# Optimization experiments

Hardware: AMD Instinct MI355X
Metric: run time of the kernel (lower is better)

The kernel has to match this reference:

```python
import jax, jax.numpy as jnp
import numpy as np

N_NODES = 100000
N_EDGES = 3200000


def setup_inputs() -> dict:
    key = jax.random.key(0)
    ks = jax.random.split(key, 5)
    features = jax.random.normal(ks[0], (N_NODES, 1433), dtype=jnp.float32)
    src = jax.random.randint(ks[1], (N_EDGES,), 0, N_NODES, dtype=jnp.int32)
    dst = jax.random.randint(ks[2], (N_EDGES,), 0, N_NODES, dtype=jnp.int32)
    # Glorot-ish init for weights
    W1 = jax.random.normal(ks[3], (1433, 16), dtype=jnp.float32) * (1.0 / np.sqrt(1433))
    W2 = jax.random.normal(ks[4], (16, 7), dtype=jnp.float32) * (1.0 / np.sqrt(16))
    b1 = jnp.zeros((16,), dtype=jnp.float32)
    b2 = jnp.zeros((7,), dtype=jnp.float32)
    return {"features": features, "src": src, "dst": dst,
            "W1": W1, "b1": b1, "W2": W2, "b2": b2}


def _degree_norms(src, dst, n_nodes, dtype):
    ones = jnp.ones(src.shape[0], dtype=dtype)
    deg_out = jax.ops.segment_sum(ones, src, num_segments=n_nodes)
    deg_in = jax.ops.segment_sum(ones, dst, num_segments=n_nodes)
    # DGL clamps zero degrees to 1
    norm_src = jax.lax.rsqrt(jnp.maximum(deg_out, 1.0))
    norm_dst = jax.lax.rsqrt(jnp.maximum(deg_in, 1.0))
    return norm_src, norm_dst


def _graph_conv(x, W, b, src, dst, norm_src, norm_dst, n_nodes):
    # DGL GraphConv, norm='both', in_feats > out_feats => weight applied first
    h = (x * norm_src[:, None]) @ W            # [N, out]
    agg = jax.ops.segment_sum(h[src], dst, num_segments=n_nodes)  # scatter-add over edges
    return agg * norm_dst[:, None] + b


def reference(features, src, dst, W1, b1, W2, b2):
    n_nodes = features.shape[0]
    norm_src, norm_dst = _degree_norms(src, dst, n_nodes, features.dtype)
    h = _graph_conv(features, W1, b1, src, dst, norm_src, norm_dst, n_nodes)
    h = jax.nn.relu(h)  # layer-1 activation (relu applied twice in original; idempotent)
    out = _graph_conv(h, W2, b2, src, dst, norm_src, norm_dst, n_nodes)
    return out
```

## Files before the change

kernel.cpp:

```cpp
#include <hip/hip_runtime.h>
#include <math.h>

#define N_NODES  100000
#define N_EDGES  3200000
#define K_IN     1433
#define NH       16
#define NO       7

#define TK       16
#define KSPLIT   9
#define CPS      10
#define RW       (CPS * TK)
#define TILE_R   128
#define SXS      20
#define NTILEV   ((N_NODES + TILE_R - 1) / TILE_R)
#define NRBV     ((NTILEV + 3) / 4)
#define SLOT     96

#define NBKT     256
#define BKN      391
#define SBLK     512
#define EPB      ((N_EDGES + SBLK - 1) / SBLK)

typedef float f4  __attribute__((ext_vector_type(4)));
typedef float f4u __attribute__((ext_vector_type(4), aligned(4)));

__global__ __launch_bounds__(256)
void k_pcount(const int* __restrict__ key, int* __restrict__ partial) {
    __shared__ int lh[NBKT];
    lh[threadIdx.x] = 0;
    __syncthreads();
    const int e0 = blockIdx.x * EPB;
    const int e1 = min(e0 + EPB, N_EDGES);
    for (int i = e0 + threadIdx.x; i < e1; i += 256)
        atomicAdd(&lh[key[i] / BKN], 1);
    __syncthreads();
    partial[blockIdx.x * NBKT + threadIdx.x] = lh[threadIdx.x];
}

__global__ __launch_bounds__(256)
void k_colscan(const int* __restrict__ partial, int* __restrict__ pbase,
               int* __restrict__ btot) {
    __shared__ int s[256];
    const int b = blockIdx.x, t = threadIdx.x;
    const int v0 = partial[(2 * t)     * NBKT + b];
    const int v1 = partial[(2 * t + 1) * NBKT + b];
    const int pair = v0 + v1;
    s[t] = pair;
    __syncthreads();
    for (int o = 1; o < 256; o <<= 1) {
        int u = (t >= o) ? s[t - o] : 0;
        __syncthreads();
        s[t] += u;
        __syncthreads();
    }
    const int excl = s[t] - pair;
    pbase[(2 * t)     * NBKT + b] = excl;
    pbase[(2 * t + 1) * NBKT + b] = excl + v0;
    if (t == 255) btot[b] = s[255];
}

__global__ __launch_bounds__(256)
void k_basescan(const int* __restrict__ btd, int* __restrict__ bbd,
                const int* __restrict__ bts, int* __restrict__ bbs) {
    __shared__ int s[256];
    const int t = threadIdx.x;
    int v = btd[t];
    s[t] = v;
    __syncthreads();
    for (int o = 1; o < 256; o <<= 1) {
        int u = (t >= o) ? s[t - o] : 0;
        __syncthreads();
        s[t] += u;
        __syncthreads();
    }
    bbd[t] = s[t] - v;
    __syncthreads();
    v = bts[t];
    s[t] = v;
    __syncthreads();
    for (int o = 1; o < 256; o <<= 1) {
        int u = (t >= o) ? s[t - o] : 0;
        __syncthreads();
        s[t] += u;
        __syncthreads();
    }
    bbs[t] = s[t] - v;
}

__global__ __launch_bounds__(256)
void k_pscatter2(const int* __restrict__ src, const int* __restrict__ dst,
                 const int* __restrict__ pbase, const int* __restrict__ bbase,
                 int2* __restrict__ ebuf) {
    __shared__ int lh[NBKT];
    __shared__ int lb[NBKT];
    const int t = threadIdx.x;
    lh[t] = 0;
    lb[t] = bbase[t] + pbase[blockIdx.x * NBKT + t];
    __syncthreads();
    const int e0 = blockIdx.x * EPB;
    const int e1 = min(e0 + EPB, N_EDGES);
    for (int i = e0 + t; i < e1; i += 256) {
        int sv = src[i], dv = dst[i];
        int b = dv / BKN;
        int p = lb[b] + atomicAdd(&lh[b], 1);
        ebuf[p] = make_int2(sv, dv);
    }
}

__global__ __launch_bounds__(256)
void k_pscatter1(const int* __restrict__ src, const int* __restrict__ pbase,
                 const int* __restrict__ bbase, int* __restrict__ sbuf) {
    __shared__ int lh[NBKT];
    __shared__ int lb[NBKT];
    const int t = threadIdx.x;
    lh[t] = 0;
    lb[t] = bbase[t] + pbase[blockIdx.x * NBKT + t];
    __syncthreads();
    const int e0 = blockIdx.x * EPB;
    const int e1 = min(e0 + EPB, N_EDGES);
    for (int i = e0 + t; i < e1; i += 256) {
        int sv = src[i];
        int b = sv / BKN;
        int p = lb[b] + atomicAdd(&lh[b], 1);
        sbuf[p] = sv;
    }
}

__global__ __launch_bounds__(512)
void k_adj(const int2* __restrict__ ebuf, const int* __restrict__ bbase,
           const int* __restrict__ btot, int* __restrict__ adj,
           int* __restrict__ cnt) {
    __shared__ int cur[BKN];
    const int b = blockIdx.x;
    for (int i = threadIdx.x; i < BKN; i += 512) cur[i] = 0;
    __syncthreads();
    const int s0 = bbase[b], s1 = s0 + btot[b];
    const int nb = b * BKN;
    for (int i = s0 + threadIdx.x; i < s1; i += 512) {
        int2 e = ebuf[i];
        int p = atomicAdd(&cur[e.y - nb], 1);
        if (p < SLOT) adj[e.y * SLOT + p] = e.x;
    }
    __syncthreads();
    for (int i = threadIdx.x; i < BKN; i += 512) {
        int n = nb + i;
        if (n < N_NODES) cnt[n] = cur[i];
    }
}

__global__ __launch_bounds__(512)
void k_hist(const int* __restrict__ sbuf, const int* __restrict__ bbase,
            const int* __restrict__ btot, int* __restrict__ deg) {
    __shared__ int cur[BKN];
    const int b = blockIdx.x;
    for (int i = threadIdx.x; i < BKN; i += 512) cur[i] = 0;
    __syncthreads();
    const int s0 = bbase[b], s1 = s0 + btot[b];
    const int nb = b * BKN;
    for (int i = s0 + threadIdx.x; i < s1; i += 512)
        atomicAdd(&cur[sbuf[i] - nb], 1);
    __syncthreads();
    for (int i = threadIdx.x; i < BKN; i += 512) {
        int n = nb + i;
        if (n < N_NODES) deg[n] = cur[i];
    }
}


#define LOADG(KN, S0,S1,S2,S3,S4,S5,S6,S7)                               \
  { if ((KN) + TK <= K_IN) {                                             \
      S0 = *(const f4u*)(xp0 + (KN)); S1 = *(const f4u*)(xp1 + (KN));    \
      S2 = *(const f4u*)(xp2 + (KN)); S3 = *(const f4u*)(xp3 + (KN));    \
      S4 = *(const f4u*)(xp4 + (KN)); S5 = *(const f4u*)(xp5 + (KN));    \
      S6 = *(const f4u*)(xp6 + (KN)); S7 = *(const f4u*)(xp7 + (KN));    \
    } else {                                                             \
      S0=0.f;S1=0.f;S2=0.f;S3=0.f;S4=0.f;S5=0.f;S6=0.f;S7=0.f;           \
      if (Lq < 2) {                                                      \
        S0 = *(const f4u*)(xp0 + (KN)); S1 = *(const f4u*)(xp1 + (KN));  \
        S2 = *(const f4u*)(xp2 + (KN)); S3 = *(const f4u*)(xp3 + (KN));  \
        S4 = *(const f4u*)(xp4 + (KN)); S5 = *(const f4u*)(xp5 + (KN));  \
        S6 = *(const f4u*)(xp6 + (KN)); S7 = *(const f4u*)(xp7 + (KN));  \
      } else if (Lq == 2) {                                              \
        S0[0] = xp0[(KN)]; S1[0] = xp1[(KN)];                            \
        S2[0] = xp2[(KN)]; S3[0] = xp3[(KN)];                            \
        S4[0] = xp4[(KN)]; S5[0] = xp5[(KN)];                            \
        S6[0] = xp6[(KN)]; S7[0] = xp7[(KN)];                            \
      }                                                                  \
    } }

#define WRITE_SET(S0,S1,S2,S3,S4,S5,S6,S7)                               \
  { *(f4*)(xbw + 0*16*SXS) = S0; *(f4*)(xbw + 1*16*SXS) = S1;            \
    *(f4*)(xbw + 2*16*SXS) = S2; *(f4*)(xbw + 3*16*SXS) = S3;            \
    *(f4*)(xbw + 4*16*SXS) = S4; *(f4*)(xbw + 5*16*SXS) = S5;            \
    *(f4*)(xbw + 6*16*SXS) = S6; *(f4*)(xbw + 7*16*SXS) = S7; }

#define READ_FMA(CC)                                                     \
  { f4 xa0 = *(const f4*)(xra +  0), xa1 = *(const f4*)(xra +  4);       \
    f4 xa2 = *(const f4*)(xra +  8), xa3 = *(const f4*)(xra + 12);       \
    f4 xb0 = *(const f4*)(xrb +  0), xb1 = *(const f4*)(xrb +  4);       \
    f4 xb2 = *(const f4*)(xrb +  8), xb3 = *(const f4*)(xrb + 12);       \
    const float* wb = wlds + (CC) * (TK * NH);                           \
    _Pragma("unroll")                                                    \
    for (int kk = 0; kk < TK; ++kk) {                                    \
      const f4 va = (kk < 4) ? xa0 : (kk < 8) ? xa1 : (kk < 12) ? xa2 : xa3; \
      const f4 vb = (kk < 4) ? xb0 : (kk < 8) ? xb1 : (kk < 12) ? xb2 : xb3; \
      const float xa = va[kk & 3], xb = vb[kk & 3];                      \
      const f4* wr = (const f4*)(wb + kk * NH);                          \
      const f4 w0 = wr[0], w1 = wr[1], w2 = wr[2], w3 = wr[3];           \
      accA0 += xa * w0; accA1 += xa * w1; accA2 += xa * w2; accA3 += xa * w3; \
      accB0 += xb * w0; accB1 += xb * w1; accB2 += xb * w2; accB3 += xb * w3; \
    } }

__global__ __launch_bounds__(256)
void k_gemm1(const float* __restrict__ X, const float* __restrict__ W1,
             float* __restrict__ hpart) {
    __shared__ float wlds[RW * NH];
    __shared__ float sX[4][TILE_R * SXS];
    const int wid = threadIdx.x >> 6;
    const int t   = threadIdx.x & 63;
    const int rb    = blockIdx.x % NRBV;
    const int split = blockIdx.x / NRBV;

    {
        const f4* W1v = (const f4*)W1;
        const int wbase = split * RW;
#pragma unroll
        for (int r = 0; r < 3; ++r) {
            int idx = r * 256 + threadIdx.x;
            if (idx < RW * 4) {
                int krow = wbase + (idx >> 2);
                f4 wv = 0.f;
                if (krow < K_IN) wv = W1v[krow * 4 + (idx & 3)];
                ((f4*)wlds)[idx] = wv;
            }
        }
    }
    __syncthreads();

    const int tile = rb * 4 + wid;
    if (tile >= NTILEV) return;
    const int base = tile * TILE_R;
    const int Lq = t & 3;
    const int Lr = t >> 2;

    const float* xp0 = X + (size_t)min(base + Lr +   0, N_NODES - 1) * K_IN + 4 * Lq;
    const float* xp1 = X + (size_t)min(base + Lr +  16, N_NODES - 1) * K_IN + 4 * Lq;
    const float* xp2 = X + (size_t)min(base + Lr +  32, N_NODES - 1) * K_IN + 4 * Lq;
    const float* xp3 = X + (size_t)min(base + Lr +  48, N_NODES - 1) * K_IN + 4 * Lq;
    const float* xp4 = X + (size_t)min(base + Lr +  64, N_NODES - 1) * K_IN + 4 * Lq;
    const float* xp5 = X + (size_t)min(base + Lr +  80, N_NODES - 1) * K_IN + 4 * Lq;
    const float* xp6 = X + (size_t)min(base + Lr +  96, N_NODES - 1) * K_IN + 4 * Lq;
    const float* xp7 = X + (size_t)min(base + Lr + 112, N_NODES - 1) * K_IN + 4 * Lq;

    float* xbuf = sX[wid];
    float* xbw  = xbuf + Lr * SXS + 4 * Lq;
    const float* xra = xbuf + t * SXS;
    const float* xrb = xbuf + (t + 64) * SXS;

    f4 accA0 = 0.f, accA1 = 0.f, accA2 = 0.f, accA3 = 0.f;
    f4 accB0 = 0.f, accB1 = 0.f, accB2 = 0.f, accB3 = 0.f;

    f4 sP0, sP1, sP2, sP3, sP4, sP5, sP6, sP7;
    f4 sQ0, sQ1, sQ2, sQ3, sQ4, sQ5, sQ6, sQ7;

    const int k0 = split * RW;
    LOADG(k0, sP0, sP1, sP2, sP3, sP4, sP5, sP6, sP7)

#pragma unroll 1
    for (int j = 0; j < CPS / 2; ++j) {
        const int ke = k0 + 2 * j * TK;
        WRITE_SET(sP0, sP1, sP2, sP3, sP4, sP5, sP6, sP7)
        LOADG(ke + TK, sQ0, sQ1, sQ2, sQ3, sQ4, sQ5, sQ6, sQ7)
        __builtin_amdgcn_wave_barrier();
        READ_FMA(2 * j)
        __builtin_amdgcn_wave_barrier();
        WRITE_SET(sQ0, sQ1, sQ2, sQ3, sQ4, sQ5, sQ6, sQ7)
        if (j + 1 < CPS / 2) {
            LOADG(ke + 2 * TK, sP0, sP1, sP2, sP3, sP4, sP5, sP6, sP7)
        }
        __builtin_amdgcn_wave_barrier();
        READ_FMA(2 * j + 1)
        __builtin_amdgcn_wave_barrier();
    }

    const size_t sb = (size_t)split * N_NODES;
    if (base + t < N_NODES) {
        f4* hp = (f4*)(hpart + (sb + base + t) * NH);
        hp[0] = accA0; hp[1] = accA1; hp[2] = accA2; hp[3] = accA3;
    }
    if (base + 64 + t < N_NODES) {
        f4* hp = (f4*)(hpart + (sb + base + 64 + t) * NH);
        hp[0] = accB0; hp[1] = accB1; hp[2] = accB2; hp[3] = accB3;
    }
}

__global__ __launch_bounds__(256)
void k_reduce(const float* __restrict__ hpart, const int* __restrict__ deg_out,
              float* __restrict__ h) {
    int idx = blockIdx.x * 256 + threadIdx.x;
    if (idx >= N_NODES * 4) return;
    f4 a = 0.f;
#pragma unroll
    for (int s = 0; s < KSPLIT; ++s)
        a += ((const f4*)hpart)[(size_t)s * N_NODES * 4 + idx];
    float ns = rsqrtf((float)max(deg_out[idx >> 2], 1));
    ((f4*)h)[idx] = a * ns;
}

__global__ __launch_bounds__(256)
void k_layer1(const float* __restrict__ h, const int* __restrict__ adj,
              const int* __restrict__ cnt, const int* __restrict__ deg_out,
              const float* __restrict__ W2, const float* __restrict__ b1,
              float* __restrict__ g) {
    const int lane = threadIdx.x & 63;
    const int wid  = threadIdx.x >> 6;
    const int d    = blockIdx.x * 4 + wid;
    if (d >= N_NODES) return;
    const int j4 = lane & 3, slot = lane >> 2;
    const int start = d * SLOT;
    const int deg   = min(cnt[d], SLOT);
    const int end   = start + deg;
    f4 agg = 0.f;
    for (int p = start + slot; p < end; p += 16) {
        int s = adj[p];
        agg += ((const f4*)h)[s * 4 + j4];
    }
#pragma unroll
    for (int off = 4; off < 64; off <<= 1) {
        agg[0] += __shfl_xor(agg[0], off);
        agg[1] += __shfl_xor(agg[1], off);
        agg[2] += __shfl_xor(agg[2], off);
        agg[3] += __shfl_xor(agg[3], off);
    }
    __shared__ float st[4][NH];
    const float nd = rsqrtf((float)max(deg, 1));
    if (slot == 0) {
        f4 bb = ((const f4*)b1)[j4];
        f4 tj;
        tj[0] = fmaxf(fmaf(agg[0], nd, bb[0]), 0.f);
        tj[1] = fmaxf(fmaf(agg[1], nd, bb[1]), 0.f);
        tj[2] = fmaxf(fmaf(agg[2], nd, bb[2]), 0.f);
        tj[3] = fmaxf(fmaf(agg[3], nd, bb[3]), 0.f);
        ((f4*)st[wid])[j4] = tj;
    }
    __builtin_amdgcn_wave_barrier();
    float r = 0.f;
    if (lane < NO) {
#pragma unroll
        for (int qq = 0; qq < NH; ++qq)
            r = fmaf(st[wid][qq], W2[qq * NO + lane], r);
    }
    if (lane < 8) {
        float ns = rsqrtf((float)max(deg_out[d], 1));
        g[(size_t)d * 8 + lane] = (lane < NO) ? ns * r : 0.f;
    }
}

__global__ __launch_bounds__(256)
void k_layer2(const float* __restrict__ g, const int* __restrict__ adj,
              const int* __restrict__ cnt, const float* __restrict__ b2,
              float* __restrict__ out) {
    const int lane = threadIdx.x & 63;
    const int wid  = threadIdx.x >> 6;
    const int d    = blockIdx.x * 4 + wid;
    if (d >= N_NODES) return;
    const int o4 = lane & 1, slot = lane >> 1;
    const int start = d * SLOT;
    const int deg   = min(cnt[d], SLOT);
    const int end   = start + deg;
    f4 agg = 0.f;
    for (int p = start + slot; p < end; p += 32) {
        int s = adj[p];
        agg += ((const f4*)g)[s * 2 + o4];
    }
#pragma unroll
    for (int off = 2; off < 64; off <<= 1) {
        agg[0] += __shfl_xor(agg[0], off);
        agg[1] += __shfl_xor(agg[1], off);
        agg[2] += __shfl_xor(agg[2], off);
        agg[3] += __shfl_xor(agg[3], off);
    }
    const int sl = lane >> 2;
    float v0 = __shfl(agg[0], sl);
    float v1 = __shfl(agg[1], sl);
    float v2 = __shfl(agg[2], sl);
    float v3 = __shfl(agg[3], sl);
    int cm = lane & 3;
    float v = (cm == 0) ? v0 : (cm == 1) ? v1 : (cm == 2) ? v2 : v3;
    if (lane < NO) {
        float nd = rsqrtf((float)max(deg, 1));
        out[(size_t)d * NO + lane] = fmaf(v, nd, b2[lane]);
    }
}

extern "C" void kernel_launch(void* const* d_in, const int* in_sizes, int n_in,
                              void* d_out, int out_size, void* d_ws, size_t ws_size,
                              hipStream_t stream) {
    const float* X   = (const float*)d_in[0];
    const int*   src = (const int*)d_in[1];
    const int*   dst = (const int*)d_in[2];
    const float* W1  = (const float*)d_in[3];
    const float* b1  = (const float*)d_in[4];
    const float* W2  = (const float*)d_in[5];
    const float* b2  = (const float*)d_in[6];
    float* out = (float*)d_out;

    char* w = (char*)d_ws;
    float* hpart    = (float*)w;  w += (size_t)KSPLIT * N_NODES * NH * 4;
    float* h        = (float*)w;  w += (size_t)N_NODES * NH * 4;
    float* g        = (float*)w;  w += (size_t)N_NODES * 8 * 4;
    int*   adj      = (int*)w;    w += (size_t)N_NODES * SLOT * 4;
    int*   deg_out_a= (int*)w;    w += (size_t)N_NODES * 4;
    int*   cnt      = (int*)w;    w += (size_t)N_NODES * 4;
    int2*  ebuf     = (int2*)w;   w += (size_t)N_EDGES * 8;
    int*   sbuf     = (int*)w;    w += (size_t)N_EDGES * 4;
    int*   partial_d= (int*)w;    w += (size_t)SBLK * NBKT * 4;
    int*   partial_s= (int*)w;    w += (size_t)SBLK * NBKT * 4;
    int*   pbase_d  = (int*)w;    w += (size_t)SBLK * NBKT * 4;
    int*   pbase_s  = (int*)w;    w += (size_t)SBLK * NBKT * 4;
    int*   btot_d   = (int*)w;    w += NBKT * 4;
    int*   btot_s   = (int*)w;    w += NBKT * 4;
    int*   bbase_d  = (int*)w;    w += NBKT * 4;
    int*   bbase_s  = (int*)w;    w += NBKT * 4;

    k_pcount   <<<SBLK, 256, 0, stream>>>(dst, partial_d);
    k_pcount   <<<SBLK, 256, 0, stream>>>(src, partial_s);
    k_colscan  <<<NBKT, 256, 0, stream>>>(partial_d, pbase_d, btot_d);
    k_colscan  <<<NBKT, 256, 0, stream>>>(partial_s, pbase_s, btot_s);
    k_basescan <<<1,    256, 0, stream>>>(btot_d, bbase_d, btot_s, bbase_s);
    k_pscatter2<<<SBLK, 256, 0, stream>>>(src, dst, pbase_d, bbase_d, ebuf);
    k_pscatter1<<<SBLK, 256, 0, stream>>>(src, pbase_s, bbase_s, sbuf);
    k_adj      <<<NBKT, 512, 0, stream>>>(ebuf, bbase_d, btot_d, adj, cnt);
    k_hist     <<<NBKT, 512, 0, stream>>>(sbuf, bbase_s, btot_s, deg_out_a);

    k_gemm1 <<<NRBV * KSPLIT, 256, 0, stream>>>(X, W1, hpart);
    k_reduce<<<(N_NODES * 4 + 255) / 256, 256, 0, stream>>>(hpart, deg_out_a, h);
    k_layer1<<<(N_NODES + 3) / 4, 256, 0, stream>>>(h, adj, cnt, deg_out_a,
                                                    W2, b1, g);
    k_layer2<<<(N_NODES + 3) / 4, 256, 0, stream>>>(g, adj, cnt, b2, out);
}
```

Measured before the change: 394.1 us.

## Restructure layer-1 GEMM tiling: 32-row wave tiles with wider K chunks

Rewrites the first-layer feature GEMM so each wave handles 32 rows, loading 64-column chunks with 16 lanes per row for more coalesced global reads. It splits the output across lanes (4 output columns per lane, 2 rows each) and changes the K split from 9 to 8 slabs of 192 columns. This should cut the partial-sum traffic the reduce kernel reads and improve the memory access pattern on the dominant 573 MB feature read. In exchange, each lane now reads more LDS per FMA, and the kernel relies on N_NODES being divisible by 32.

```diff
diff --git a/kernel.cpp b/kernel.cpp
--- a/kernel.cpp
+++ b/kernel.cpp
@@ -7,14 +7,12 @@
 #define NH       16
 #define NO       7
 
-#define TK       16
-#define KSPLIT   9
-#define CPS      10
-#define RW       (CPS * TK)
-#define TILE_R   128
-#define SXS      20
-#define NTILEV   ((N_NODES + TILE_R - 1) / TILE_R)
-#define NRBV     ((NTILEV + 3) / 4)
+#define TR2      32
+#define NT2      (N_NODES / TR2)
+#define NRB2     ((NT2 + 3) / 4)
+#define KS2      8
+#define RW2      192
+#define SX2      68
 #define SLOT     96
 
 #define NBKT     256
@@ -168,131 +166,127 @@
 }
 
 
-#define LOADG(KN, S0,S1,S2,S3,S4,S5,S6,S7)                               \
-  { if ((KN) + TK <= K_IN) {                                             \
-      S0 = *(const f4u*)(xp0 + (KN)); S1 = *(const f4u*)(xp1 + (KN));    \
-      S2 = *(const f4u*)(xp2 + (KN)); S3 = *(const f4u*)(xp3 + (KN));    \
-      S4 = *(const f4u*)(xp4 + (KN)); S5 = *(const f4u*)(xp5 + (KN));    \
-      S6 = *(const f4u*)(xp6 + (KN)); S7 = *(const f4u*)(xp7 + (KN));    \
-    } else {                                                             \
-      S0=0.f;S1=0.f;S2=0.f;S3=0.f;S4=0.f;S5=0.f;S6=0.f;S7=0.f;           \
-      if (Lq < 2) {                                                      \
-        S0 = *(const f4u*)(xp0 + (KN)); S1 = *(const f4u*)(xp1 + (KN));  \
-        S2 = *(const f4u*)(xp2 + (KN)); S3 = *(const f4u*)(xp3 + (KN));  \
-        S4 = *(const f4u*)(xp4 + (KN)); S5 = *(const f4u*)(xp5 + (KN));  \
-        S6 = *(const f4u*)(xp6 + (KN)); S7 = *(const f4u*)(xp7 + (KN));  \
-      } else if (Lq == 2) {                                              \
-        S0[0] = xp0[(KN)]; S1[0] = xp1[(KN)];                            \
-        S2[0] = xp2[(KN)]; S3[0] = xp3[(KN)];                            \
-        S4[0] = xp4[(KN)]; S5[0] = xp5[(KN)];                            \
-        S6[0] = xp6[(KN)]; S7[0] = xp7[(KN)];                            \
-      }                                                                  \
+#define LOADX_FULL(KO, S0,S1,S2,S3,S4,S5,S6,S7)                      \
+  { S0 = *(const f4u*)(xrow + 0*4*K_IN + (KO));                      \
+    S1 = *(const f4u*)(xrow + 1*4*K_IN + (KO));                      \
+    S2 = *(const f4u*)(xrow + 2*4*K_IN + (KO));                      \
+    S3 = *(const f4u*)(xrow + 3*4*K_IN + (KO));                      \
+    S4 = *(const f4u*)(xrow + 4*4*K_IN + (KO));                      \
+    S5 = *(const f4u*)(xrow + 5*4*K_IN + (KO));                      \
+    S6 = *(const f4u*)(xrow + 6*4*K_IN + (KO));                      \
+    S7 = *(const f4u*)(xrow + 7*4*K_IN + (KO)); }
+
+#define LOADX_TAIL(KO, S0,S1,S2,S3,S4,S5,S6,S7)                      \
+  { S0=0.f;S1=0.f;S2=0.f;S3=0.f;S4=0.f;S5=0.f;S6=0.f;S7=0.f;         \
+    const int kl_ = (KO) + 4 * Lq;                                   \
+    if (kl_ + 3 < K_IN) {                                            \
+      LOADX_FULL(KO, S0,S1,S2,S3,S4,S5,S6,S7)                        \
+    } else {                                                         \
+      _Pragma("unroll")                                              \
+      for (int m_ = 0; m_ < 4; ++m_)                                 \
+        if (kl_ + m_ < K_IN) {                                       \
+          S0[m_] = xrow[0*4*K_IN + (KO) + m_];                       \
+          S1[m_] = xrow[1*4*K_IN + (KO) + m_];                       \
+          S2[m_] = xrow[2*4*K_IN + (KO) + m_];                       \
+          S3[m_] = xrow[3*4*K_IN + (KO) + m_];                       \
+          S4[m_] = xrow[4*4*K_IN + (KO) + m_];                       \
+          S5[m_] = xrow[5*4*K_IN + (KO) + m_];                       \
+          S6[m_] = xrow[6*4*K_IN + (KO) + m_];                       \
+          S7[m_] = xrow[7*4*K_IN + (KO) + m_];                       \
+        }                                                            \
     } }
 
-#define WRITE_SET(S0,S1,S2,S3,S4,S5,S6,S7)                               \
-  { *(f4*)(xbw + 0*16*SXS) = S0; *(f4*)(xbw + 1*16*SXS) = S1;            \
-    *(f4*)(xbw + 2*16*SXS) = S2; *(f4*)(xbw + 3*16*SXS) = S3;            \
-    *(f4*)(xbw + 4*16*SXS) = S4; *(f4*)(xbw + 5*16*SXS) = S5;            \
-    *(f4*)(xbw + 6*16*SXS) = S6; *(f4*)(xbw + 7*16*SXS) = S7; }
-
-#define READ_FMA(CC)                                                     \
-  { f4 xa0 = *(const f4*)(xra +  0), xa1 = *(const f4*)(xra +  4);       \
-    f4 xa2 = *(const f4*)(xra +  8), xa3 = *(const f4*)(xra + 12);       \
-    f4 xb0 = *(const f4*)(xrb +  0), xb1 = *(const f4*)(xrb +  4);       \
-    f4 xb2 = *(const f4*)(xrb +  8), xb3 = *(const f4*)(xrb + 12);       \
-    const float* wb = wlds + (CC) * (TK * NH);                           \
-    _Pragma("unroll")                                                    \
-    for (int kk = 0; kk < TK; ++kk) {                                    \
-      const f4 va = (kk < 4) ? xa0 : (kk < 8) ? xa1 : (kk < 12) ? xa2 : xa3; \
-      const f4 vb = (kk < 4) ? xb0 : (kk < 8) ? xb1 : (kk < 12) ? xb2 : xb3; \
-      const float xa = va[kk & 3], xb = vb[kk & 3];                      \
-      const f4* wr = (const f4*)(wb + kk * NH);                          \
-      const f4 w0 = wr[0], w1 = wr[1], w2 = wr[2], w3 = wr[3];           \
-      accA0 += xa * w0; accA1 += xa * w1; accA2 += xa * w2; accA3 += xa * w3; \
-      accB0 += xb * w0; accB1 += xb * w1; accB2 += xb * w2; accB3 += xb * w3; \
+#define LOADX(KO, S0,S1,S2,S3,S4,S5,S6,S7)                           \
+  { if ((KO) + 64 <= K_IN) { LOADX_FULL(KO, S0,S1,S2,S3,S4,S5,S6,S7) } \
+    else                   { LOADX_TAIL(KO, S0,S1,S2,S3,S4,S5,S6,S7) } }
+
+#define WRX(S0,S1,S2,S3,S4,S5,S6,S7)                                 \
+  { *(f4*)(xbw + 0*4*SX2) = S0; *(f4*)(xbw + 1*4*SX2) = S1;          \
+    *(f4*)(xbw + 2*4*SX2) = S2; *(f4*)(xbw + 3*4*SX2) = S3;          \
+    *(f4*)(xbw + 4*4*SX2) = S4; *(f4*)(xbw + 5*4*SX2) = S5;          \
+    *(f4*)(xbw + 6*4*SX2) = S6; *(f4*)(xbw + 7*4*SX2) = S7; }
+
+#define CFMA(GOFF)                                                   \
+  { const float* wb = wjq + (GOFF) * NH;                             \
+    _Pragma("unroll")                                                \
+    for (int kq = 0; kq < 16; ++kq) {                                \
+      f4 xA = *(const f4*)(xrdA + kq * 4);                           \
+      f4 xB = *(const f4*)(xrdB + kq * 4);                           \
+      f4 w0 = *(const f4*)(wb + (kq*4+0) * NH);                      \
+      f4 w1 = *(const f4*)(wb + (kq*4+1) * NH);                      \
+      f4 w2 = *(const f4*)(wb + (kq*4+2) * NH);                      \
+      f4 w3 = *(const f4*)(wb + (kq*4+3) * NH);                      \
+      acc0 += xA[0]*w0; acc0 += xA[1]*w1;                            \
+      acc0 += xA[2]*w2; acc0 += xA[3]*w3;                            \
+      acc1 += xB[0]*w0; acc1 += xB[1]*w1;                            \
+      acc1 += xB[2]*w2; acc1 += xB[3]*w3;                            \
     } }
 
 __global__ __launch_bounds__(256)
 void k_gemm1(const float* __restrict__ X, const float* __restrict__ W1,
              float* __restrict__ hpart) {
-    __shared__ float wlds[RW * NH];
-    __shared__ float sX[4][TILE_R * SXS];
+    __shared__ float wlds[RW2 * NH];
+    __shared__ float sX[4][TR2 * SX2];
     const int wid = threadIdx.x >> 6;
     const int t   = threadIdx.x & 63;
-    const int rb    = blockIdx.x % NRBV;
-    const int split = blockIdx.x / NRBV;
+    const int rb    = blockIdx.x % NRB2;
+    const int split = blockIdx.x / NRB2;
 
     {
         const f4* W1v = (const f4*)W1;
-        const int wbase = split * RW;
+        const int wbase = split * RW2;
 #pragma unroll
         for (int r = 0; r < 3; ++r) {
             int idx = r * 256 + threadIdx.x;
-            if (idx < RW * 4) {
-                int krow = wbase + (idx >> 2);
-                f4 wv = 0.f;
-                if (krow < K_IN) wv = W1v[krow * 4 + (idx & 3)];
-                ((f4*)wlds)[idx] = wv;
-            }
+            int krow = wbase + (idx >> 2);
+            f4 wv = 0.f;
+            if (krow < K_IN) wv = W1v[krow * 4 + (idx & 3)];
+            ((f4*)wlds)[idx] = wv;
         }
     }
     __syncthreads();
 
     const int tile = rb * 4 + wid;
-    if (tile >= NTILEV) return;
-    const int base = tile * TILE_R;
-    const int Lq = t & 3;
-    const int Lr = t >> 2;
-
-    const float* xp0 = X + (size_t)min(base + Lr +   0, N_NODES - 1) * K_IN + 4 * Lq;
-    const float* xp1 = X + (size_t)min(base + Lr +  16, N_NODES - 1) * K_IN + 4 * Lq;
-    const float* xp2 = X + (size_t)min(base + Lr +  32, N_NODES - 1) * K_IN + 4 * Lq;
-    const float* xp3 = X + (size_t)min(base + Lr +  48, N_NODES - 1) * K_IN + 4 * Lq;
-    const float* xp4 = X + (size_t)min(base + Lr +  64, N_NODES - 1) * K_IN + 4 * Lq;
-    const float* xp5 = X + (size_t)min(base + Lr +  80, N_NODES - 1) * K_IN + 4 * Lq;
-    const float* xp6 = X + (size_t)min(base + Lr +  96, N_NODES - 1) * K_IN + 4 * Lq;
-    const float* xp7 = X + (size_t)min(base + Lr + 112, N_NODES - 1) * K_IN + 4 * Lq;
+    if (tile >= NT2) return;
+    const int base = tile * TR2;
+    const int Lq = t & 15;
+    const int Lr = t >> 4;
+    const int rg = t >> 2;
+    const int jq = t & 3;
+
+    const float* xrow = X + (size_t)(base + Lr) * K_IN + 4 * Lq;
 
     float* xbuf = sX[wid];
-    float* xbw  = xbuf + Lr * SXS + 4 * Lq;
-    const float* xra = xbuf + t * SXS;
-    const float* xrb = xbuf + (t + 64) * SXS;
-
-    f4 accA0 = 0.f, accA1 = 0.f, accA2 = 0.f, accA3 = 0.f;
-    f4 accB0 = 0.f, accB1 = 0.f, accB2 = 0.f, accB3 = 0.f;
-
-    f4 sP0, sP1, sP2, sP3, sP4, sP5, sP6, sP7;
-    f4 sQ0, sQ1, sQ2, sQ3, sQ4, sQ5, sQ6, sQ7;
-
-    const int k0 = split * RW;
-    LOADG(k0, sP0, sP1, sP2, sP3, sP4, sP5, sP6, sP7)
-
-#pragma unroll 1
-    for (int j = 0; j < CPS / 2; ++j) {
-        const int ke = k0 + 2 * j * TK;
-        WRITE_SET(sP0, sP1, sP2, sP3, sP4, sP5, sP6, sP7)
-        LOADG(ke + TK, sQ0, sQ1, sQ2, sQ3, sQ4, sQ5, sQ6, sQ7)
-        __builtin_amdgcn_wave_barrier();
-        READ_FMA(2 * j)
-        __builtin_amdgcn_wave_barrier();
-        WRITE_SET(sQ0, sQ1, sQ2, sQ3, sQ4, sQ5, sQ6, sQ7)
-        if (j + 1 < CPS / 2) {
-            LOADG(ke + 2 * TK, sP0, sP1, sP2, sP3, sP4, sP5, sP6, sP7)
-        }
-        __builtin_amdgcn_wave_barrier();
-        READ_FMA(2 * j + 1)
-        __builtin_amdgcn_wave_barrier();
-    }
+    float* xbw  = xbuf + Lr * SX2 + 4 * Lq;
+    const float* xrdA = xbuf + rg * SX2;
+    const float* xrdB = xbuf + (rg + 16) * SX2;
+    const float* wjq  = wlds + jq * 4;
+
+    f4 acc0 = 0.f, acc1 = 0.f;
+    f4 P0, P1, P2, P3, P4, P5, P6, P7;
+    f4 Q0, Q1, Q2, Q3, Q4, Q5, Q6, Q7;
+
+    const int kb = split * RW2;
+
+    LOADX(kb +   0, P0, P1, P2, P3, P4, P5, P6, P7)
+    WRX(P0, P1, P2, P3, P4, P5, P6, P7)
+    LOADX(kb +  64, Q0, Q1, Q2, Q3, Q4, Q5, Q6, Q7)
+    __builtin_amdgcn_wave_barrier();
+    CFMA(0)
+    __builtin_amdgcn_wave_barrier();
+    WRX(Q0, Q1, Q2, Q3, Q4, Q5, Q6, Q7)
+    LOADX(kb + 128, P0, P1, P2, P3, P4, P5, P6, P7)
+    __builtin_amdgcn_wave_barrier();
+    CFMA(64)
+    __builtin_amdgcn_wave_barrier();
+    WRX(P0, P1, P2, P3, P4, P5, P6, P7)
+    __builtin_amdgcn_wave_barrier();
+    CFMA(128)
 
     const size_t sb = (size_t)split * N_NODES;
-    if (base + t < N_NODES) {
-        f4* hp = (f4*)(hpart + (sb + base + t) * NH);
-        hp[0] = accA0; hp[1] = accA1; hp[2] = accA2; hp[3] = accA3;
-    }
-    if (base + 64 + t < N_NODES) {
-        f4* hp = (f4*)(hpart + (sb + base + 64 + t) * NH);
-        hp[0] = accB0; hp[1] = accB1; hp[2] = accB2; hp[3] = accB3;
-    }
+    float* op = hpart + (sb + base + rg) * NH + jq * 4;
+    *(f4*)op = acc0;
+    *(f4*)(op + (size_t)16 * NH) = acc1;
 }
 
 __global__ __launch_bounds__(256)
@@ -302,7 +296,7 @@
     if (idx >= N_NODES * 4) return;
     f4 a = 0.f;
 #pragma unroll
-    for (int s = 0; s < KSPLIT; ++s)
+    for (int s = 0; s < KS2; ++s)
         a += ((const f4*)hpart)[(size_t)s * N_NODES * 4 + idx];
     float ns = rsqrtf((float)max(deg_out[idx >> 2], 1));
     ((f4*)h)[idx] = a * ns;
@@ -407,7 +401,7 @@
     float* out = (float*)d_out;
 
     char* w = (char*)d_ws;
-    float* hpart    = (float*)w;  w += (size_t)KSPLIT * N_NODES * NH * 4;
+    float* hpart    = (float*)w;  w += (size_t)KS2 * N_NODES * NH * 4;
     float* h        = (float*)w;  w += (size_t)N_NODES * NH * 4;
     float* g        = (float*)w;  w += (size_t)N_NODES * 8 * 4;
     int*   adj      = (int*)w;    w += (size_t)N_NODES * SLOT * 4;
@@ -434,7 +428,7 @@
     k_adj      <<<NBKT, 512, 0, stream>>>(ebuf, bbase_d, btot_d, adj, cnt);
     k_hist     <<<NBKT, 512, 0, stream>>>(sbuf, bbase_s, btot_s, deg_out_a);
 
-    k_gemm1 <<<NRBV * KSPLIT, 256, 0, stream>>>(X, W1, hpart);
+    k_gemm1 <<<NRB2 * KS2, 256, 0, stream>>>(X, W1, hpart);
     k_reduce<<<(N_NODES * 4 + 255) / 256, 256, 0, stream>>>(hpart, deg_out_a, h);
     k_layer1<<<(N_NODES + 3) / 4, 256, 0, stream>>>(h, adj, cnt, deg_out_a,
                                                     W2, b1, g);
```

New measurement: 415.2 us. +5.4%, slower.
